# Performance work log

Hardware: AMD Instinct MI355X
Metric: run time of the kernel (lower is better)

Reference implementation:

```python
import jax, jax.numpy as jnp
import numpy as np
from jax import lax

EPS = 1e-5

def conv2d(x, w, groups=1, pad=0):
    return lax.conv_general_dilated(
        x, w, window_strides=(1, 1), padding=[(pad, pad), (pad, pad)],
        dimension_numbers=('NCHW', 'OIHW', 'NCHW'), feature_group_count=groups)

def setup_inputs() -> dict:
    key = jax.random.key(0)
    ks = jax.random.split(key, 10)
    B, C, H, W = 8, 64, 128, 128
    s = 0.05
    f32 = jnp.float32
    return {
        'x': jax.random.normal(ks[0], (B, C, H, W), f32),
        # key_embed: Conv2d(64,64,3,groups=8,bias=False) -> weight [64, 64/8, 3, 3]
        'w_key': jax.random.normal(ks[1], (64, 8, 3, 3), f32) * s,
        # embed[0]: Conv2d(128,32,1,groups=2,bias=False) -> [32, 128/2, 1, 1]
        'w_e1': jax.random.normal(ks[2], (32, 64, 1, 1), f32) * s,
        # embed[2]: Conv2d(32,72,1,groups=2,bias=True) -> [72, 32/2, 1, 1]
        'w_e2': jax.random.normal(ks[3], (72, 16, 1, 1), f32) * s,
        'b_e2': jax.random.normal(ks[4], (72,), f32) * s,
        # GroupNorm(num_groups=8, num_channels=72) affine params
        'gn_w': jnp.ones((72,), f32),
        'gn_b': jnp.zeros((72,), f32),
        # conv1x1: Conv2d(64,64,1,groups=2,bias=False) -> [64, 32, 1, 1]
        'w_c1': jax.random.normal(ks[5], (64, 32, 1, 1), f32) * s,
        # conv_du: Conv2d(64,4,1,bias=False), Conv2d(4,64,1,bias=False)
        'w_du1': jax.random.normal(ks[6], (4, 64, 1, 1), f32) * s,
        'w_du2': jax.random.normal(ks[7], (64, 4, 1, 1), f32) * s,
    }

def reference(x, w_key, w_e1, w_e2, b_e2, gn_w, gn_b, w_c1, w_du1, w_du2):
    B, C, H, W = x.shape  # C == 64
    KK = 9                # kernel_size^2
    # key embedding: grouped 3x3 conv + ReLU
    k = jax.nn.relu(conv2d(x, w_key, groups=8, pad=1))
    # interleave x and k along channels: view of [B,64,2,H,W] -> [B,128,H,W]
    qk = jnp.stack([x, k], axis=2).reshape(B, 2 * C, H, W)
    # dynamic kernel generation (embed)
    w = jax.nn.relu(conv2d(qk, w_e1, groups=2))
    w = conv2d(w, w_e2, groups=2) + b_e2[None, :, None, None]  # [B,72,H,W]
    # GroupNorm(8, 72): normalize over (channels-in-group, H, W)
    wg = w.reshape(B, 8, 9, H, W)
    m = wg.mean(axis=(2, 3, 4), keepdims=True)
    v = wg.var(axis=(2, 3, 4), keepdims=True)
    w = ((wg - m) * lax.rsqrt(v + EPS)).reshape(B, 72, H, W)
    w = w * gn_w[None, :, None, None] + gn_b[None, :, None, None]
    # per-pixel kernels: [B*2, 4, 9, H, W]
    w = w.reshape(B * 2, 4, KK, H, W)
    # value path
    xv = conv2d(x, w_c1, groups=2).reshape(B * 2, 32, H, W)
    # unfold 3x3 patches with zero padding 1 -> [B*2, 32, 9, H, W]
    xp = jnp.pad(xv, ((0, 0), (0, 0), (1, 1), (1, 1)))
    patches = jnp.stack(
        [xp[:, :, i:i + H, j:j + W] for i in range(3) for j in range(3)], axis=2)
    # share_planes=8: 8 channels share each kernel -> [B*2, 4, 8, 9, H, W]
    patches = patches.reshape(B * 2, 4, 8, KK, H, W)
    out = jnp.einsum('bgckhw,bgkhw->bgchw', patches, w)  # local conv
    out = out.reshape(B, C, H, W)
    # channel attention
    y = out.mean(axis=(2, 3))                 # [B, 64]
    y = jax.nn.relu(y @ w_du1[:, :, 0, 0].T)  # [B, 4]
    y = jax.nn.sigmoid(y @ w_du2[:, :, 0, 0].T)  # [B, 64]
    return out * y[:, :, None, None]
```

## Files before the change

kernel.cpp:

```cpp
#include <hip/hip_runtime.h>
#include <math.h>

#define Hd 128
#define Wd 128
#define HW 16384

__device__ __forceinline__ float wred(float v) {
  #pragma unroll
  for (int o = 32; o > 0; o >>= 1) v += __shfl_down(v, o, 64);
  return v;
}

__global__ __launch_bounds__(256) void k_keyconv(const float* __restrict__ x,
                                                 const float* __restrict__ wkey,
                                                 float* __restrict__ kout) {
  __shared__ float xt[8][18][24];
  const int tid = threadIdx.x;
  const int tx = tid & 15, ty = tid >> 4;
  const int b = blockIdx.z >> 3, g = blockIdx.z & 7;
  const int h0 = blockIdx.y * 16, w0 = blockIdx.x * 16;
  const int h = h0 + ty, w = w0 + tx;
  for (int i = tid; i < 8 * 324; i += 256) {
    int ch = i / 324, r = i - ch * 324;
    int yy = r / 18, xx = r - yy * 18;
    int gh = h0 + yy - 1, gw = w0 + xx - 1;
    float v = 0.f;
    if (gh >= 0 && gh < Hd && gw >= 0 && gw < Wd)
      v = x[((long)(b * 64 + g * 8 + ch) << 14) + (gh << 7) + gw];
    xt[ch][yy][xx] = v;
  }
  __syncthreads();
  float acc[8] = {0.f, 0.f, 0.f, 0.f, 0.f, 0.f, 0.f, 0.f};
  const float* wg = wkey + g * 576;
  #pragma unroll
  for (int i = 0; i < 8; ++i) {
    float nb[9];
    #pragma unroll
    for (int dy = 0; dy < 3; ++dy)
      #pragma unroll
      for (int dx = 0; dx < 3; ++dx)
        nb[dy * 3 + dx] = xt[i][ty + dy][tx + dx];
    #pragma unroll
    for (int oc = 0; oc < 8; ++oc) {
      const float* wr = wg + oc * 72 + i * 9;
      #pragma unroll
      for (int t = 0; t < 9; ++t) acc[oc] += wr[t] * nb[t];
    }
  }
  #pragma unroll
  for (int oc = 0; oc < 8; ++oc)
    kout[((long)(b * 64 + g * 8 + oc) << 14) + (h << 7) + w] = fmaxf(acc[oc], 0.f);
}

__global__ __launch_bounds__(256) void k_embed(const float* __restrict__ x,
                                               float* __restrict__ kxv,
                                               const float* __restrict__ we1,
                                               const float* __restrict__ we2,
                                               const float* __restrict__ be2,
                                               const float* __restrict__ wc1,
                                               float* __restrict__ wpre,
                                               float* __restrict__ spart) {
  const int tid = threadIdx.x;
  const int p = blockIdx.x * 256 + tid;
  const int b = blockIdx.y;
  const int s = blockIdx.z;
  float xc[32], kc[32];
  #pragma unroll
  for (int j = 0; j < 32; ++j) {
    xc[j] = x[((long)(b * 64 + 32 * s + j) << 14) + p];
    kc[j] = kxv[((long)(b * 64 + 32 * s + j) << 14) + p];
  }
  #pragma unroll 4
  for (int o = 0; o < 32; ++o) {
    const float* wr = wc1 + (32 * s + o) * 32;
    float a = 0.f;
    #pragma unroll
    for (int j = 0; j < 32; ++j) a += wr[j] * xc[j];
    kxv[((long)(b * 64 + 32 * s + o) << 14) + p] = a;
  }
  float w1a[16];
  #pragma unroll
  for (int o = 0; o < 16; ++o) {
    const float* wr = we1 + (16 * s + o) * 64;
    float a = 0.f;
    #pragma unroll
    for (int j = 0; j < 32; ++j) a += wr[2 * j] * xc[j] + wr[2 * j + 1] * kc[j];
    w1a[o] = fmaxf(a, 0.f);
  }
  const int row = blockIdx.x * 4 + (tid >> 6);
  #pragma unroll
  for (int gl = 0; gl < 4; ++gl) {
    float lgs = 0.f, lgq = 0.f;
    #pragma unroll
    for (int kk = 0; kk < 9; ++kk) {
      const int oc2 = 36 * s + gl * 9 + kk;
      const float* wr = we2 + oc2 * 16;
      float a = be2[oc2];
      #pragma unroll
      for (int ic = 0; ic < 16; ++ic) a += wr[ic] * w1a[ic];
      wpre[((long)(b * 72 + oc2) << 14) + p] = a;
      lgs += a;
      lgq += a * a;
    }
    float r1 = wred(lgs), r2 = wred(lgq);
    if ((tid & 63) == 0) {
      spart[row * 128 + (b * 8 + 4 * s + gl) * 2 + 0] = r1;
      spart[row * 128 + (b * 8 + 4 * s + gl) * 2 + 1] = r2;
    }
  }
}

__global__ void k_gnstat(const float* __restrict__ spart, float* __restrict__ minv) {
  __shared__ float sred[128];
  const int t = threadIdx.x;
  float a = 0.f;
  #pragma unroll 8
  for (int r = 0; r < 256; ++r) a += spart[r * 128 + t];
  sred[t] = a;
  __syncthreads();
  if (t < 64) {
    const float N = 9.f * (float)HW;
    float s = sred[2 * t], q = sred[2 * t + 1];
    float m = s / N;
    float var = q / N - m * m;
    minv[2 * t] = m;
    minv[2 * t + 1] = rsqrtf(var + 1e-5f);
  }
}

__global__ __launch_bounds__(256) void k_local(const float* __restrict__ kxv,
                                               const float* __restrict__ wpre,
                                               const float* __restrict__ minv,
                                               const float* __restrict__ gnw,
                                               const float* __restrict__ gnb,
                                               float* __restrict__ out,
                                               float* __restrict__ part) {
  __shared__ float xt[8][18][24];
  const int tid = threadIdx.x;
  const int tx = tid & 15, ty = tid >> 4;
  const int z = blockIdx.z;
  const int b2 = z >> 2, g = z & 3;
  const int t = b2 & 1, b = b2 >> 1;
  const int h0 = blockIdx.y * 16, w0 = blockIdx.x * 16;
  const int tileid = blockIdx.y * 8 + blockIdx.x;
  const int p = ((h0 + ty) << 7) + (w0 + tx);
  for (int i = tid; i < 8 * 324; i += 256) {
    int ch = i / 324, r = i - ch * 324;
    int yy = r / 18, xx = r - yy * 18;
    int gh = h0 + yy - 1, gw = w0 + xx - 1;
    float v = 0.f;
    if (gh >= 0 && gh < Hd && gw >= 0 && gw < Wd)
      v = kxv[((long)(b2 * 32 + g * 8 + ch) << 14) + (gh << 7) + gw];
    xt[ch][yy][xx] = v;
  }
  __syncthreads();
  const int gg = 4 * t + g;
  const float m = minv[(b * 8 + gg) * 2];
  const float inv = minv[(b * 8 + gg) * 2 + 1];
  float wn[9];
  #pragma unroll
  for (int kk = 0; kk < 9; ++kk) {
    const int ch72 = 36 * t + 9 * g + kk;
    float wv = wpre[((long)(b * 72 + ch72) << 14) + p];
    wn[kk] = (wv - m) * inv * gnw[ch72] + gnb[ch72];
  }
  const int prow = tileid * 4 + (tid >> 6);
  #pragma unroll
  for (int cc = 0; cc < 8; ++cc) {
    float o = 0.f;
    #pragma unroll
    for (int dy = 0; dy < 3; ++dy)
      #pragma unroll
      for (int dx = 0; dx < 3; ++dx)
        o += wn[dy * 3 + dx] * xt[cc][ty + dy][tx + dx];
    const int ch512 = b2 * 32 + g * 8 + cc;
    out[((long)ch512 << 14) + p] = o;
    float os = wred(o);
    if ((tid & 63) == 0) part[prow * 512 + ch512] = os;
  }
}

__global__ void k_ca(const float* __restrict__ part, const float* __restrict__ du1,
                     const float* __restrict__ du2, float* __restrict__ ys) {
  __shared__ float sy[8][64];
  __shared__ float sy4[8][4];
  const int tid = threadIdx.x;
  const int b = tid >> 6, c = tid & 63;
  float acc = 0.f;
  #pragma unroll 8
  for (int r = 0; r < 256; ++r) acc += part[r * 512 + tid];
  sy[b][c] = acc * (1.f / (float)HW);
  __syncthreads();
  if (tid < 32) {
    int bb = tid >> 2, j = tid & 3;
    float a = 0.f;
    for (int c2 = 0; c2 < 64; ++c2) a += sy[bb][c2] * du1[j * 64 + c2];
    sy4[bb][j] = fmaxf(a, 0.f);
  }
  __syncthreads();
  float z = 0.f;
  #pragma unroll
  for (int j = 0; j < 4; ++j) z += sy4[b][j] * du2[c * 4 + j];
  ys[tid] = 1.f / (1.f + expf(-z));
}

__global__ __launch_bounds__(256) void k_scale(float* __restrict__ out,
                                               const float* __restrict__ ys) {
  const long i4 = (long)blockIdx.x * 256 + threadIdx.x;
  const long e = i4 * 4;
  const int bc = (int)(e >> 14);
  const float s = ys[bc];
  float4* o = (float4*)out;
  float4 v = o[i4];
  v.x *= s; v.y *= s; v.z *= s; v.w *= s;
  o[i4] = v;
}

extern "C" void kernel_launch(void* const* d_in, const int* in_sizes, int n_in,
                              void* d_out, int out_size, void* d_ws, size_t ws_size,
                              hipStream_t stream) {
  const float* x    = (const float*)d_in[0];
  const float* wkey = (const float*)d_in[1];
  const float* we1  = (const float*)d_in[2];
  const float* we2  = (const float*)d_in[3];
  const float* be2  = (const float*)d_in[4];
  const float* gnw  = (const float*)d_in[5];
  const float* gnb  = (const float*)d_in[6];
  const float* wc1  = (const float*)d_in[7];
  const float* du1  = (const float*)d_in[8];
  const float* du2  = (const float*)d_in[9];
  float* out = (float*)d_out;
  float* ws = (float*)d_ws;

  float* kxv  = ws;
  float* wpre = ws + 8388608;
  float* part = ws + 17825792;
  float* spart = part;
  float* minv = part + 131072;
  float* ys   = minv + 128;

  k_keyconv<<<dim3(8, 8, 64), 256, 0, stream>>>(x, wkey, kxv);
  k_embed<<<dim3(64, 8, 2), 256, 0, stream>>>(x, kxv, we1, we2, be2, wc1, wpre, spart);
  k_gnstat<<<1, 128, 0, stream>>>(spart, minv);
  k_local<<<dim3(8, 8, 64), 256, 0, stream>>>(kxv, wpre, minv, gnw, gnb, out, part);
  k_ca<<<1, 512, 0, stream>>>(part, du1, du2, ys);
  k_scale<<<8192, 256, 0, stream>>>(out, ys);
}
```

Before: 247.1 us.

## Compute two output rows per thread in conv kernels and split embed work

In the grouped 3x3 key conv and the local-conv kernel, each thread now produces two vertically adjacent pixels. The shared tile grows to 34 rows, so one 4x3 neighbourhood load feeds both outputs and fewer shared-memory reads are needed per output. The embed kernel now covers 128 pixels per block, and the two thread halves divide the value-conv channels and GroupNorm groups between them. A barrier protects the in-place overwrite of kxv. The price is duplicated input loads and a duplicated first embed layer, higher register pressure, and half as many blocks for the conv kernels.

```diff
diff --git a/kernel.cpp b/kernel.cpp
--- a/kernel.cpp
+++ b/kernel.cpp
@@ -14,14 +14,13 @@
 __global__ __launch_bounds__(256) void k_keyconv(const float* __restrict__ x,
                                                  const float* __restrict__ wkey,
                                                  float* __restrict__ kout) {
-  __shared__ float xt[8][18][24];
+  __shared__ float xt[8][34][24];
   const int tid = threadIdx.x;
   const int tx = tid & 15, ty = tid >> 4;
   const int b = blockIdx.z >> 3, g = blockIdx.z & 7;
-  const int h0 = blockIdx.y * 16, w0 = blockIdx.x * 16;
-  const int h = h0 + ty, w = w0 + tx;
-  for (int i = tid; i < 8 * 324; i += 256) {
-    int ch = i / 324, r = i - ch * 324;
+  const int h0 = blockIdx.y * 32, w0 = blockIdx.x * 16;
+  for (int i = tid; i < 8 * 612; i += 256) {
+    int ch = i / 612, r = i - ch * 612;
     int yy = r / 18, xx = r - yy * 18;
     int gh = h0 + yy - 1, gw = w0 + xx - 1;
     float v = 0.f;
@@ -30,26 +29,37 @@
     xt[ch][yy][xx] = v;
   }
   __syncthreads();
-  float acc[8] = {0.f, 0.f, 0.f, 0.f, 0.f, 0.f, 0.f, 0.f};
+  float acc0[8] = {0.f, 0.f, 0.f, 0.f, 0.f, 0.f, 0.f, 0.f};
+  float acc1[8] = {0.f, 0.f, 0.f, 0.f, 0.f, 0.f, 0.f, 0.f};
   const float* wg = wkey + g * 576;
   #pragma unroll
-  for (int i = 0; i < 8; ++i) {
-    float nb[9];
-    #pragma unroll
-    for (int dy = 0; dy < 3; ++dy)
-      #pragma unroll
-      for (int dx = 0; dx < 3; ++dx)
-        nb[dy * 3 + dx] = xt[i][ty + dy][tx + dx];
+  for (int ich = 0; ich < 8; ++ich) {
+    float nb[12];
+    #pragma unroll
+    for (int rr = 0; rr < 4; ++rr)
+      #pragma unroll
+      for (int cc = 0; cc < 3; ++cc)
+        nb[rr * 3 + cc] = xt[ich][2 * ty + rr][tx + cc];
     #pragma unroll
     for (int oc = 0; oc < 8; ++oc) {
-      const float* wr = wg + oc * 72 + i * 9;
-      #pragma unroll
-      for (int t = 0; t < 9; ++t) acc[oc] += wr[t] * nb[t];
+      const float* wr = wg + oc * 72 + ich * 9;
+      #pragma unroll
+      for (int dy = 0; dy < 3; ++dy)
+        #pragma unroll
+        for (int dx = 0; dx < 3; ++dx) {
+          float wv = wr[dy * 3 + dx];
+          acc0[oc] += wv * nb[dy * 3 + dx];
+          acc1[oc] += wv * nb[(dy + 1) * 3 + dx];
+        }
     }
   }
-  #pragma unroll
-  for (int oc = 0; oc < 8; ++oc)
-    kout[((long)(b * 64 + g * 8 + oc) << 14) + (h << 7) + w] = fmaxf(acc[oc], 0.f);
+  const int h = h0 + 2 * ty, w = w0 + tx;
+  #pragma unroll
+  for (int oc = 0; oc < 8; ++oc) {
+    const long base = ((long)(b * 64 + g * 8 + oc) << 14);
+    kout[base + (h << 7) + w] = fmaxf(acc0[oc], 0.f);
+    kout[base + ((h + 1) << 7) + w] = fmaxf(acc1[oc], 0.f);
+  }
 }
 
 __global__ __launch_bounds__(256) void k_embed(const float* __restrict__ x,
@@ -61,7 +71,9 @@
                                                float* __restrict__ wpre,
                                                float* __restrict__ spart) {
   const int tid = threadIdx.x;
-  const int p = blockIdx.x * 256 + tid;
+  const int half = tid >> 7;
+  const int q = tid & 127;
+  const int p = blockIdx.x * 128 + q;
   const int b = blockIdx.y;
   const int s = blockIdx.z;
   float xc[32], kc[32];
@@ -70,8 +82,10 @@
     xc[j] = x[((long)(b * 64 + 32 * s + j) << 14) + p];
     kc[j] = kxv[((long)(b * 64 + 32 * s + j) << 14) + p];
   }
+  __syncthreads();
   #pragma unroll 4
-  for (int o = 0; o < 32; ++o) {
+  for (int oo = 0; oo < 16; ++oo) {
+    const int o = 16 * half + oo;
     const float* wr = wc1 + (32 * s + o) * 32;
     float a = 0.f;
     #pragma unroll
@@ -87,9 +101,10 @@
     for (int j = 0; j < 32; ++j) a += wr[2 * j] * xc[j] + wr[2 * j + 1] * kc[j];
     w1a[o] = fmaxf(a, 0.f);
   }
-  const int row = blockIdx.x * 4 + (tid >> 6);
-  #pragma unroll
-  for (int gl = 0; gl < 4; ++gl) {
+  const int row = blockIdx.x * 2 + ((tid >> 6) & 1);
+  #pragma unroll
+  for (int gi = 0; gi < 2; ++gi) {
+    const int gl = 2 * half + gi;
     float lgs = 0.f, lgq = 0.f;
     #pragma unroll
     for (int kk = 0; kk < 9; ++kk) {
@@ -135,17 +150,15 @@
                                                const float* __restrict__ gnb,
                                                float* __restrict__ out,
                                                float* __restrict__ part) {
-  __shared__ float xt[8][18][24];
+  __shared__ float xt[8][34][24];
   const int tid = threadIdx.x;
   const int tx = tid & 15, ty = tid >> 4;
   const int z = blockIdx.z;
   const int b2 = z >> 2, g = z & 3;
   const int t = b2 & 1, b = b2 >> 1;
-  const int h0 = blockIdx.y * 16, w0 = blockIdx.x * 16;
-  const int tileid = blockIdx.y * 8 + blockIdx.x;
-  const int p = ((h0 + ty) << 7) + (w0 + tx);
-  for (int i = tid; i < 8 * 324; i += 256) {
-    int ch = i / 324, r = i - ch * 324;
+  const int h0 = blockIdx.y * 32, w0 = blockIdx.x * 16;
+  for (int i = tid; i < 8 * 612; i += 256) {
+    int ch = i / 612, r = i - ch * 612;
     int yy = r / 18, xx = r - yy * 18;
     int gh = h0 + yy - 1, gw = w0 + xx - 1;
     float v = 0.f;
@@ -157,25 +170,38 @@
   const int gg = 4 * t + g;
   const float m = minv[(b * 8 + gg) * 2];
   const float inv = minv[(b * 8 + gg) * 2 + 1];
-  float wn[9];
+  const int p0 = ((h0 + 2 * ty) << 7) + (w0 + tx);
+  const int p1 = p0 + 128;
+  float wn0[9], wn1[9];
   #pragma unroll
   for (int kk = 0; kk < 9; ++kk) {
     const int ch72 = 36 * t + 9 * g + kk;
-    float wv = wpre[((long)(b * 72 + ch72) << 14) + p];
-    wn[kk] = (wv - m) * inv * gnw[ch72] + gnb[ch72];
-  }
-  const int prow = tileid * 4 + (tid >> 6);
+    const long base = ((long)(b * 72 + ch72) << 14);
+    const float sc = inv * gnw[ch72], sh = gnb[ch72] - m * inv * gnw[ch72];
+    wn0[kk] = wpre[base + p0] * sc + sh;
+    wn1[kk] = wpre[base + p1] * sc + sh;
+  }
+  const int prow = (blockIdx.y * 8 + blockIdx.x) * 4 + (tid >> 6);
   #pragma unroll
   for (int cc = 0; cc < 8; ++cc) {
-    float o = 0.f;
+    float nb[12];
+    #pragma unroll
+    for (int rr = 0; rr < 4; ++rr)
+      #pragma unroll
+      for (int ccol = 0; ccol < 3; ++ccol)
+        nb[rr * 3 + ccol] = xt[cc][2 * ty + rr][tx + ccol];
+    float o0 = 0.f, o1 = 0.f;
     #pragma unroll
     for (int dy = 0; dy < 3; ++dy)
       #pragma unroll
-      for (int dx = 0; dx < 3; ++dx)
-        o += wn[dy * 3 + dx] * xt[cc][ty + dy][tx + dx];
+      for (int dx = 0; dx < 3; ++dx) {
+        o0 += wn0[dy * 3 + dx] * nb[dy * 3 + dx];
+        o1 += wn1[dy * 3 + dx] * nb[(dy + 1) * 3 + dx];
+      }
     const int ch512 = b2 * 32 + g * 8 + cc;
-    out[((long)ch512 << 14) + p] = o;
-    float os = wred(o);
+    out[((long)ch512 << 14) + p0] = o0;
+    out[((long)ch512 << 14) + p1] = o1;
+    float os = wred(o0 + o1);
     if ((tid & 63) == 0) part[prow * 512 + ch512] = os;
   }
 }
@@ -188,7 +214,7 @@
   const int b = tid >> 6, c = tid & 63;
   float acc = 0.f;
   #pragma unroll 8
-  for (int r = 0; r < 256; ++r) acc += part[r * 512 + tid];
+  for (int r = 0; r < 128; ++r) acc += part[r * 512 + tid];
   sy[b][c] = acc * (1.f / (float)HW);
   __syncthreads();
   if (tid < 32) {
@@ -239,10 +265,10 @@
   float* minv = part + 131072;
   float* ys   = minv + 128;
 
-  k_keyconv<<<dim3(8, 8, 64), 256, 0, stream>>>(x, wkey, kxv);
-  k_embed<<<dim3(64, 8, 2), 256, 0, stream>>>(x, kxv, we1, we2, be2, wc1, wpre, spart);
+  k_keyconv<<<dim3(8, 4, 64), 256, 0, stream>>>(x, wkey, kxv);
+  k_embed<<<dim3(128, 8, 2), 256, 0, stream>>>(x, kxv, we1, we2, be2, wc1, wpre, spart);
   k_gnstat<<<1, 128, 0, stream>>>(spart, minv);
-  k_local<<<dim3(8, 8, 64), 256, 0, stream>>>(kxv, wpre, minv, gnw, gnb, out, part);
+  k_local<<<dim3(8, 4, 64), 256, 0, stream>>>(kxv, wpre, minv, gnw, gnb, out, part);
   k_ca<<<1, 512, 0, stream>>>(part, du1, du2, ys);
   k_scale<<<8192, 256, 0, stream>>>(out, ys);
 }
```

Result: slower. 286.0 us (+15.7%).
